# Kernel tuning notes

Measured on AMD Instinct MI355X. Metric: run time of the kernel, lower is better.

Reference implementation:

```python
import jax, jax.numpy as jnp
import numpy as np

C, H, W, N = 256, 256, 256, 512
ROI_SIZE = 7


def setup_inputs() -> dict:
    key = jax.random.key(0)
    k1, k2, k3 = jax.random.split(key, 3)
    feature = jax.random.normal(k1, (C, H, W), dtype=jnp.float32)
    # rois layout: (y1, x1, y2, x2), valid boxes inside the map
    start = jax.random.uniform(k2, (N, 2), jnp.float32, 0.0, H / 2)
    size = jax.random.uniform(k3, (N, 2), jnp.float32, 8.0, H / 2)
    rois = jnp.concatenate([start, start + size], axis=-1)
    return {"feature": feature, "rois": rois}


def _bilinear(feature, x, y):
    # feature: [C, H, W]; x, y: [...] float sample coords.
    # Faithful to the torch code: corners are clamped BEFORE computing the
    # interpolation weights (y - y1, y2 - y, etc.).
    h, w = feature.shape[-2:]
    y1 = jnp.floor(y).astype(jnp.int32)
    y2 = y1 + 1
    x1 = jnp.floor(x).astype(jnp.int32)
    x2 = x1 + 1
    y1 = jnp.clip(y1, 0, h - 1)
    y2 = jnp.clip(y2, 0, h - 1)
    x1 = jnp.clip(x1, 0, w - 1)
    x2 = jnp.clip(x2, 0, w - 1)
    wy1 = y - y1  # dist to top (clamped) corner
    wy2 = y2 - y
    wx1 = x - x1
    wx2 = x2 - x
    f11 = feature[:, y1, x1]  # [C, ...]
    f12 = feature[:, y1, x2]
    f21 = feature[:, y2, x1]
    f22 = feature[:, y2, x2]
    p = f11 * wx2 + f12 * wx1
    q = f21 * wx2 + f22 * wx1
    return p * wy2 + q * wy1


def reference(feature, rois):
    # feature: [C, H, W]; rois: [N, 4] = (y1, x1, y2, x2)
    R = ROI_SIZE
    n_roi = rois.shape[0]
    c = feature.shape[0]
    stride_h = (rois[:, 2] - rois[:, 0]) / R  # [N]
    stride_w = (rois[:, 3] - rois[:, 1]) / R  # [N]
    bins = jnp.arange(R, dtype=feature.dtype)
    y_base = rois[:, 0, None] + stride_h[:, None] * bins  # [N, 7]
    x_base = rois[:, 1, None] + stride_w[:, None] * bins  # [N, 7]
    # two sample points per bin, at 1/3 and 2/3 of the bin stride
    ys = jnp.stack([y_base + stride_h[:, None] / 3,
                    y_base + 2 * stride_h[:, None] / 3], axis=-1)  # [N, 7, 2]
    xs = jnp.stack([x_base + stride_w[:, None] / 3,
                    x_base + 2 * stride_w[:, None] / 3], axis=-1)  # [N, 7, 2]
    # all (y_sample, x_sample) combos per (roi, bin_m, bin_n): [N, 7, 7, 2, 2]
    Y = ys[:, :, None, :, None]
    X = xs[:, None, :, None, :]
    Yb, Xb = jnp.broadcast_arrays(Y, X)
    vals = _bilinear(feature, Xb, Yb)  # [C, N, 7, 7, 2, 2]
    # Faithful to torch.max(cat(...)) on a [C, 4] tensor: a GLOBAL max over
    # both channels and the 4 sample points, broadcast back to all channels.
    pooled = vals.max(axis=(0, -2, -1))  # [N, 7, 7]
    return jnp.broadcast_to(pooled[:, None, :, :], (n_roi, c, R, R))
```

## Files before the change

kernel.cpp:

```cpp
#include <hip/hip_runtime.h>

#define CCH 256
#define HH  256
#define WW  256
#define HWSZ (HH * WW)
#define NROI 512
#define RBIN 7
#define NBIN (RBIN * RBIN)
#define TFEAT_BYTES ((size_t)HWSZ * CCH * 2)

typedef float vfloat2 __attribute__((ext_vector_type(2)));

__device__ __forceinline__ unsigned short f2bf_rne(float f) {
    unsigned u = __float_as_uint(f);
    u = (u + 0x7fffu + ((u >> 16) & 1u)) >> 16;
    return (unsigned short)u;
}
__device__ __forceinline__ float bf2f(unsigned short h) {
    return __uint_as_float(((unsigned)h) << 16);
}

__global__ __launch_bounds__(256)
void transpose_chw_to_hwc_bf16(const float* __restrict__ feat,
                               unsigned short* __restrict__ tfeat)
{
    __shared__ float tile[32][65];
    const int t   = threadIdx.x;
    const int hw0 = blockIdx.x * 64;
    const int c0  = blockIdx.y * 32;

    #pragma unroll
    for (int j = 0; j < 4; ++j) {
        const int cl = (t >> 5) + j * 8;
        const int hl = (t & 31) * 2;
        const vfloat2 v = __builtin_nontemporal_load(
            (const vfloat2*)(feat + (size_t)(c0 + cl) * HWSZ + hw0 + hl));
        tile[cl][hl]     = v.x;
        tile[cl][hl + 1] = v.y;
    }
    __syncthreads();
    #pragma unroll
    for (int j = 0; j < 4; ++j) {
        const int hl = (t >> 4) + j * 16;
        const int cl = (t & 15) * 2;
        ushort2 w;
        w.x = f2bf_rne(tile[cl][hl]);
        w.y = f2bf_rne(tile[cl + 1][hl]);
        *(ushort2*)(tfeat + (size_t)(hw0 + hl) * CCH + c0 + cl) = w;
    }
}

__global__ __launch_bounds__(1024)
void roialign_fused(const unsigned short* __restrict__ tfeat,
                    const float* __restrict__ rois,
                    float* __restrict__ out)
{
    const int n    = blockIdx.x;
    const int t    = threadIdx.x;
    const int wave = t >> 6;
    const int lane = t & 63;

    __shared__ float pmax[196];
    __shared__ float pooled[NBIN];

    const float y0 = rois[n * 4 + 0];
    const float x0 = rois[n * 4 + 1];
    const float sh = (rois[n * 4 + 2] - y0) / (float)RBIN;
    const float sw = (rois[n * 4 + 3] - x0) / (float)RBIN;

    for (int p = wave; p < 196; p += 16) {
        const int py = p / 14;
        const int px = p % 14;
        const int by = py >> 1, sy = py & 1;
        const int bx = px >> 1, sx = px & 1;

        const float y = y0 + sh * (float)by +
                        ((sy == 0) ? (sh / 3.0f) : (2.0f * sh / 3.0f));
        const float x = x0 + sw * (float)bx +
                        ((sx == 0) ? (sw / 3.0f) : (2.0f * sw / 3.0f));

        int iy1 = (int)floorf(y);
        int iy2 = iy1 + 1;
        int ix1 = (int)floorf(x);
        int ix2 = ix1 + 1;
        iy1 = min(max(iy1, 0), HH - 1);
        iy2 = min(max(iy2, 0), HH - 1);
        ix1 = min(max(ix1, 0), WW - 1);
        ix2 = min(max(ix2, 0), WW - 1);

        const float wy1 = y - (float)iy1;
        const float wy2 = (float)iy2 - y;
        const float wx1 = x - (float)ix1;
        const float wx2 = (float)ix2 - x;

        const ushort4 a = ((const ushort4*)(tfeat + (size_t)(iy1 * WW + ix1) * CCH))[lane];
        const ushort4 b = ((const ushort4*)(tfeat + (size_t)(iy1 * WW + ix2) * CCH))[lane];
        const ushort4 c = ((const ushort4*)(tfeat + (size_t)(iy2 * WW + ix1) * CCH))[lane];
        const ushort4 d = ((const ushort4*)(tfeat + (size_t)(iy2 * WW + ix2) * CCH))[lane];

        float m;
        {
            float pp, qq, v0, v1;
            pp = bf2f(a.x) * wx2 + bf2f(b.x) * wx1;
            qq = bf2f(c.x) * wx2 + bf2f(d.x) * wx1;
            v0 = pp * wy2 + qq * wy1;
            pp = bf2f(a.y) * wx2 + bf2f(b.y) * wx1;
            qq = bf2f(c.y) * wx2 + bf2f(d.y) * wx1;
            v1 = pp * wy2 + qq * wy1;
            m = fmaxf(v0, v1);
            pp = bf2f(a.z) * wx2 + bf2f(b.z) * wx1;
            qq = bf2f(c.z) * wx2 + bf2f(d.z) * wx1;
            v0 = pp * wy2 + qq * wy1;
            pp = bf2f(a.w) * wx2 + bf2f(b.w) * wx1;
            qq = bf2f(c.w) * wx2 + bf2f(d.w) * wx1;
            v1 = pp * wy2 + qq * wy1;
            m = fmaxf(m, fmaxf(v0, v1));
        }

        #pragma unroll
        for (int off = 32; off > 0; off >>= 1)
            m = fmaxf(m, __shfl_xor(m, off, 64));

        if (lane == 0) pmax[p] = m;
    }
    __syncthreads();

    if (t < NBIN) {
        const int by = t / RBIN, bx = t % RBIN;
        const int p00 = (2 * by) * 14 + 2 * bx;
        pooled[t] = fmaxf(fmaxf(pmax[p00],      pmax[p00 + 1]),
                          fmaxf(pmax[p00 + 14], pmax[p00 + 15]));
    }
    __syncthreads();

    float* o = out + (size_t)n * (CCH * NBIN);
    #pragma unroll
    for (int k = 0; k < 13; ++k) {
        const int idx = t + k * 1024;
        if (idx < CCH * NBIN)
            __builtin_nontemporal_store(pooled[idx % NBIN], o + idx);
    }
}

__global__ __launch_bounds__(256)
void roialign_direct_kernel(const float* __restrict__ feat,
                            const float* __restrict__ rois,
                            float* __restrict__ out)
{
    const int n = blockIdx.x;
    const int t = threadIdx.x;
    __shared__ float ptmax[196];
    __shared__ float pooled[NBIN];

    const float y0  = rois[n * 4 + 0];
    const float x0  = rois[n * 4 + 1];
    const float sh  = (rois[n * 4 + 2] - y0) / (float)RBIN;
    const float sw  = (rois[n * 4 + 3] - x0) / (float)RBIN;

    const bool active = (t < 196);
    int off11 = 0, off12 = 0, off21 = 0, off22 = 0;
    float wx1 = 0.f, wx2 = 0.f, wy1 = 0.f, wy2 = 0.f;
    if (active) {
        const int py = t / 14, px = t % 14;
        const int by = py >> 1, sy = py & 1;
        const int bx = px >> 1, sx = px & 1;
        const float y = y0 + sh * (float)by + ((sy == 0) ? (sh / 3.0f) : (2.0f * sh / 3.0f));
        const float x = x0 + sw * (float)bx + ((sx == 0) ? (sw / 3.0f) : (2.0f * sw / 3.0f));
        int iy1 = (int)floorf(y), iy2 = iy1 + 1;
        int ix1 = (int)floorf(x), ix2 = ix1 + 1;
        iy1 = min(max(iy1, 0), HH - 1); iy2 = min(max(iy2, 0), HH - 1);
        ix1 = min(max(ix1, 0), WW - 1); ix2 = min(max(ix2, 0), WW - 1);
        wy1 = y - (float)iy1; wy2 = (float)iy2 - y;
        wx1 = x - (float)ix1; wx2 = (float)ix2 - x;
        off11 = iy1 * WW + ix1; off12 = iy1 * WW + ix2;
        off21 = iy2 * WW + ix1; off22 = iy2 * WW + ix2;
    }
    if (active) {
        float m = -INFINITY;
        const float* f = feat;
        #pragma unroll 4
        for (int c = 0; c < CCH; ++c) {
            const float p = f[off11] * wx2 + f[off12] * wx1;
            const float q = f[off21] * wx2 + f[off22] * wx1;
            m = fmaxf(m, p * wy2 + q * wy1);
            f += HWSZ;
        }
        ptmax[t] = m;
    }
    __syncthreads();
    if (t < NBIN) {
        const int by = t / RBIN, bx = t % RBIN;
        const int p00 = (2 * by) * 14 + 2 * bx;
        pooled[t] = fmaxf(fmaxf(ptmax[p00], ptmax[p00 + 1]),
                          fmaxf(ptmax[p00 + 14], ptmax[p00 + 15]));
    }
    __syncthreads();
    float* o = out + (size_t)n * (CCH * NBIN);
    for (int idx = t; idx < CCH * NBIN; idx += 256)
        o[idx] = pooled[idx % NBIN];
}

extern "C" void kernel_launch(void* const* d_in, const int* in_sizes, int n_in,
                              void* d_out, int out_size, void* d_ws, size_t ws_size,
                              hipStream_t stream)
{
    const float* feat = (const float*)d_in[0];
    const float* rois = (const float*)d_in[1];
    float* out = (float*)d_out;

    if (ws_size < TFEAT_BYTES) {
        roialign_direct_kernel<<<NROI, 256, 0, stream>>>(feat, rois, out);
        return;
    }

    unsigned short* tfeat = (unsigned short*)d_ws;

    dim3 tgrid(HWSZ / 64, CCH / 32);
    transpose_chw_to_hwc_bf16<<<tgrid, 256, 0, stream>>>(feat, tfeat);

    roialign_fused<<<NROI, 1024, 0, stream>>>(tfeat, rois, out);
}
```

Measured before the change: 135.7 us.

## Widen transpose tiles and remap RoI sampling to one wave per bin

The transpose kernel now handles 64x64 tiles with 16-byte float4 loads and 8-byte bf16 stores, so each block moves more data with fewer, wider memory operations. The fused RoI kernel assigns one wave per output bin instead of one per sample point. Each half-wave covers two of the four sample points, and each lane loads 8 channels per corner with 16-byte loads. This removes the intermediate shared-memory pass and reduces the number of loop iterations and shuffle reductions. The trade-off is more registers per thread and lower wave utilisation, since 49 bins are spread over 16 waves.

Result: faster. 131.8 us (-2.8%).

```diff
diff --git a/kernel.cpp b/kernel.cpp
--- a/kernel.cpp
+++ b/kernel.cpp
@@ -9,44 +9,45 @@
 #define NBIN (RBIN * RBIN)
 #define TFEAT_BYTES ((size_t)HWSZ * CCH * 2)
 
-typedef float vfloat2 __attribute__((ext_vector_type(2)));
+typedef float vfloat4 __attribute__((ext_vector_type(4)));
 
 __device__ __forceinline__ unsigned short f2bf_rne(float f) {
     unsigned u = __float_as_uint(f);
     u = (u + 0x7fffu + ((u >> 16) & 1u)) >> 16;
     return (unsigned short)u;
 }
-__device__ __forceinline__ float bf2f(unsigned short h) {
-    return __uint_as_float(((unsigned)h) << 16);
-}
 
 __global__ __launch_bounds__(256)
 void transpose_chw_to_hwc_bf16(const float* __restrict__ feat,
                                unsigned short* __restrict__ tfeat)
 {
-    __shared__ float tile[32][65];
+    __shared__ float tile[64][65];
     const int t   = threadIdx.x;
     const int hw0 = blockIdx.x * 64;
-    const int c0  = blockIdx.y * 32;
+    const int c0  = blockIdx.y * 64;
 
     #pragma unroll
     for (int j = 0; j < 4; ++j) {
-        const int cl = (t >> 5) + j * 8;
-        const int hl = (t & 31) * 2;
-        const vfloat2 v = __builtin_nontemporal_load(
-            (const vfloat2*)(feat + (size_t)(c0 + cl) * HWSZ + hw0 + hl));
+        const int cl = (t >> 4) + j * 16;
+        const int hl = (t & 15) * 4;
+        const vfloat4 v = __builtin_nontemporal_load(
+            (const vfloat4*)(feat + (size_t)(c0 + cl) * HWSZ + hw0 + hl));
         tile[cl][hl]     = v.x;
         tile[cl][hl + 1] = v.y;
+        tile[cl][hl + 2] = v.z;
+        tile[cl][hl + 3] = v.w;
     }
     __syncthreads();
     #pragma unroll
     for (int j = 0; j < 4; ++j) {
         const int hl = (t >> 4) + j * 16;
-        const int cl = (t & 15) * 2;
-        ushort2 w;
+        const int cl = (t & 15) * 4;
+        ushort4 w;
         w.x = f2bf_rne(tile[cl][hl]);
         w.y = f2bf_rne(tile[cl + 1][hl]);
-        *(ushort2*)(tfeat + (size_t)(hw0 + hl) * CCH + c0 + cl) = w;
+        w.z = f2bf_rne(tile[cl + 2][hl]);
+        w.w = f2bf_rne(tile[cl + 3][hl]);
+        *(ushort4*)(tfeat + (size_t)(hw0 + hl) * CCH + c0 + cl) = w;
     }
 }
 
@@ -59,8 +60,9 @@
     const int t    = threadIdx.x;
     const int wave = t >> 6;
     const int lane = t & 63;
-
-    __shared__ float pmax[196];
+    const int half = lane >> 5;
+    const int cOff = (lane & 31) * 8;
+
     __shared__ float pooled[NBIN];
 
     const float y0 = rois[n * 4 + 0];
@@ -68,68 +70,80 @@
     const float sh = (rois[n * 4 + 2] - y0) / (float)RBIN;
     const float sw = (rois[n * 4 + 3] - x0) / (float)RBIN;
 
-    for (int p = wave; p < 196; p += 16) {
-        const int py = p / 14;
-        const int px = p % 14;
-        const int by = py >> 1, sy = py & 1;
-        const int bx = px >> 1, sx = px & 1;
-
-        const float y = y0 + sh * (float)by +
-                        ((sy == 0) ? (sh / 3.0f) : (2.0f * sh / 3.0f));
-        const float x = x0 + sw * (float)bx +
-                        ((sx == 0) ? (sw / 3.0f) : (2.0f * sw / 3.0f));
-
-        int iy1 = (int)floorf(y);
-        int iy2 = iy1 + 1;
-        int ix1 = (int)floorf(x);
-        int ix2 = ix1 + 1;
-        iy1 = min(max(iy1, 0), HH - 1);
-        iy2 = min(max(iy2, 0), HH - 1);
-        ix1 = min(max(ix1, 0), WW - 1);
-        ix2 = min(max(ix2, 0), WW - 1);
-
-        const float wy1 = y - (float)iy1;
-        const float wy2 = (float)iy2 - y;
-        const float wx1 = x - (float)ix1;
-        const float wx2 = (float)ix2 - x;
-
-        const ushort4 a = ((const ushort4*)(tfeat + (size_t)(iy1 * WW + ix1) * CCH))[lane];
-        const ushort4 b = ((const ushort4*)(tfeat + (size_t)(iy1 * WW + ix2) * CCH))[lane];
-        const ushort4 c = ((const ushort4*)(tfeat + (size_t)(iy2 * WW + ix1) * CCH))[lane];
-        const ushort4 d = ((const ushort4*)(tfeat + (size_t)(iy2 * WW + ix2) * CCH))[lane];
-
-        float m;
-        {
-            float pp, qq, v0, v1;
-            pp = bf2f(a.x) * wx2 + bf2f(b.x) * wx1;
-            qq = bf2f(c.x) * wx2 + bf2f(d.x) * wx1;
-            v0 = pp * wy2 + qq * wy1;
-            pp = bf2f(a.y) * wx2 + bf2f(b.y) * wx1;
-            qq = bf2f(c.y) * wx2 + bf2f(d.y) * wx1;
-            v1 = pp * wy2 + qq * wy1;
-            m = fmaxf(v0, v1);
-            pp = bf2f(a.z) * wx2 + bf2f(b.z) * wx1;
-            qq = bf2f(c.z) * wx2 + bf2f(d.z) * wx1;
-            v0 = pp * wy2 + qq * wy1;
-            pp = bf2f(a.w) * wx2 + bf2f(b.w) * wx1;
-            qq = bf2f(c.w) * wx2 + bf2f(d.w) * wx1;
-            v1 = pp * wy2 + qq * wy1;
-            m = fmaxf(m, fmaxf(v0, v1));
+    for (int bin = wave; bin < NBIN; bin += 16) {
+        const int by = bin / RBIN;
+        const int bx = bin % RBIN;
+
+        float acc[8];
+        #pragma unroll
+        for (int k = 0; k < 8; ++k) acc[k] = -INFINITY;
+
+        #pragma unroll
+        for (int i = 0; i < 2; ++i) {
+            const int point = i * 2 + half;
+            const int sy = point >> 1;
+            const int sx = point & 1;
+
+            const float y = y0 + sh * (float)by +
+                            ((sy == 0) ? (sh / 3.0f) : (2.0f * sh / 3.0f));
+            const float x = x0 + sw * (float)bx +
+                            ((sx == 0) ? (sw / 3.0f) : (2.0f * sw / 3.0f));
+
+            int iy1 = (int)floorf(y);
+            int iy2 = iy1 + 1;
+            int ix1 = (int)floorf(x);
+            int ix2 = ix1 + 1;
+            iy1 = min(max(iy1, 0), HH - 1);
+            iy2 = min(max(iy2, 0), HH - 1);
+            ix1 = min(max(ix1, 0), WW - 1);
+            ix2 = min(max(ix2, 0), WW - 1);
+
+            const float wy1 = y - (float)iy1;
+            const float wy2 = (float)iy2 - y;
+            const float wx1 = x - (float)ix1;
+            const float wx2 = (float)ix2 - x;
+
+            const uint4 A = *(const uint4*)(tfeat + (size_t)(iy1 * WW + ix1) * CCH + cOff);
+            const uint4 B = *(const uint4*)(tfeat + (size_t)(iy1 * WW + ix2) * CCH + cOff);
+            const uint4 C = *(const uint4*)(tfeat + (size_t)(iy2 * WW + ix1) * CCH + cOff);
+            const uint4 D = *(const uint4*)(tfeat + (size_t)(iy2 * WW + ix2) * CCH + cOff);
+            const unsigned* ap = (const unsigned*)&A;
+            const unsigned* bp = (const unsigned*)&B;
+            const unsigned* cp = (const unsigned*)&C;
+            const unsigned* dp = (const unsigned*)&D;
+
+            #pragma unroll
+            for (int k = 0; k < 4; ++k) {
+                const unsigned ua = ap[k], ub = bp[k], uc = cp[k], ud = dp[k];
+                {
+                    const float f11 = __uint_as_float(ua << 16);
+                    const float f12 = __uint_as_float(ub << 16);
+                    const float f21 = __uint_as_float(uc << 16);
+                    const float f22 = __uint_as_float(ud << 16);
+                    const float p = f11 * wx2 + f12 * wx1;
+                    const float q = f21 * wx2 + f22 * wx1;
+                    acc[2 * k] = fmaxf(acc[2 * k], p * wy2 + q * wy1);
+                }
+                {
+                    const float f11 = __uint_as_float(ua & 0xffff0000u);
+                    const float f12 = __uint_as_float(ub & 0xffff0000u);
+                    const float f21 = __uint_as_float(uc & 0xffff0000u);
+                    const float f22 = __uint_as_float(ud & 0xffff0000u);
+                    const float p = f11 * wx2 + f12 * wx1;
+                    const float q = f21 * wx2 + f22 * wx1;
+                    acc[2 * k + 1] = fmaxf(acc[2 * k + 1], p * wy2 + q * wy1);
+                }
+            }
         }
+
+        float m = fmaxf(fmaxf(fmaxf(acc[0], acc[1]), fmaxf(acc[2], acc[3])),
+                        fmaxf(fmaxf(acc[4], acc[5]), fmaxf(acc[6], acc[7])));
 
         #pragma unroll
         for (int off = 32; off > 0; off >>= 1)
             m = fmaxf(m, __shfl_xor(m, off, 64));
 
-        if (lane == 0) pmax[p] = m;
-    }
-    __syncthreads();
-
-    if (t < NBIN) {
-        const int by = t / RBIN, bx = t % RBIN;
-        const int p00 = (2 * by) * 14 + 2 * bx;
-        pooled[t] = fmaxf(fmaxf(pmax[p00],      pmax[p00 + 1]),
-                          fmaxf(pmax[p00 + 14], pmax[p00 + 15]));
+        if (lane == 0) pooled[bin] = m;
     }
     __syncthreads();
 
@@ -215,7 +229,7 @@
 
     unsigned short* tfeat = (unsigned short*)d_ws;
 
-    dim3 tgrid(HWSZ / 64, CCH / 32);
+    dim3 tgrid(HWSZ / 64, CCH / 64);
     transpose_chw_to_hwc_bf16<<<tgrid, 256, 0, stream>>>(feat, tfeat);
 
     roialign_fused<<<NROI, 1024, 0, stream>>>(tfeat, rois, out);
```
